# Kernel tuning notes

Measured on AMD Instinct MI355X. Metric: run time of the kernel, lower is better.

## Reference

```python
import jax, jax.numpy as jnp
import numpy as np

B, T, D = 4, 2048, 1024
E, H, K = 8, 2048, 2  # n_expert, expert_dim, top_k


def setup_inputs() -> dict:
    key = jax.random.key(0)
    k1, k2, k3, k4 = jax.random.split(key, 4)
    x = jax.random.normal(k1, (B, T, D), jnp.float32)
    gate_w = jax.random.normal(k2, (D, E), jnp.float32) * 0.02          # Router gate (no bias)
    w1 = jax.random.normal(k3, (E, D, H), jnp.float32) * (1.0 / np.sqrt(D))  # per-expert first Linear
    w2 = jax.random.normal(k4, (E, H, D), jnp.float32) * (1.0 / np.sqrt(H))  # per-expert second Linear
    return {"x": x, "gate_w": gate_w, "w1": w1, "w2": w2}


def reference(x, gate_w, w1, w2):
    b, t, d = x.shape
    xf = x.reshape(-1, d)                                   # [N, D]
    n = xf.shape[0]
    n_expert = gate_w.shape[1]
    # Router
    logits = xf @ gate_w                                    # [N, E]
    probs = jax.nn.softmax(logits, axis=-1)
    topk_probs, topk_idx = jax.lax.top_k(probs, K)          # [N, K]
    topk_probs = topk_probs / jnp.sum(topk_probs, axis=-1, keepdims=True)
    # Dense compute of ALL experts (faithful to original), then gather top-k
    h = jax.nn.gelu(jnp.einsum('nd,edh->neh', xf, w1), approximate=False)  # [N, E, H]
    all_expert_out = jnp.einsum('neh,ehd->ned', h, w2)      # [N, E, D]
    selected = jnp.take_along_axis(all_expert_out, topk_idx[:, :, None], axis=1)  # [N, K, D]
    out = jnp.sum(topk_probs[:, :, None] * selected, axis=1)  # [N, D]  (dropout p=0 -> identity)
    # Load-balancing aux loss
    counts = jnp.zeros((n_expert,), jnp.float32).at[topk_idx.reshape(-1)].add(1.0)
    tokens_per_expert = counts / n
    mean_probs = jnp.mean(probs, axis=0)
    aux_loss = n_expert * jnp.sum(tokens_per_expert * mean_probs)
    return (out.reshape(b, t, d), aux_loss,
            probs.reshape(b, t, n_expert),
            topk_idx.reshape(b, t, K),
            topk_probs.reshape(b, t, K))
```

## Files before the change

### kernel.cpp

```cpp
#include <hip/hip_runtime.h>
#include <hip/hip_bf16.h>
#include <cstdint>

typedef unsigned short u16;
typedef unsigned int u32;
typedef short s16x8 __attribute__((ext_vector_type(8)));
typedef float f32x4 __attribute__((ext_vector_type(4)));

constexpr int NTOK = 8192;
constexpr int DDIM = 1024;
constexpr int NEXP = 8;
constexpr int HDIM = 2048;
constexpr int NPAIR = NTOK * 2;

constexpr size_t OFF_OUT   = 0;
constexpr size_t OFF_AUX   = 8388608;
constexpr size_t OFF_PROBS = 8388609;
constexpr size_t OFF_TIDX  = 8454145;
constexpr size_t OFF_TPR   = 8470529;

constexpr size_t WS_CNT  = 0;
constexpr size_t WS_PSUM = 32;
constexpr size_t WS_IDS  = 1024;
constexpr size_t WS_PRW  = 263168;
constexpr size_t WS_W1T  = 17302528;
constexpr size_t WS_W2T  = 50856960;
constexpr size_t WS_H    = 84411392;
constexpr size_t WS_XB   = 151520256;
constexpr size_t WS_NEED = 168297472;

__device__ __forceinline__ u16 f2b(float f) {
  u32 u = __float_as_uint(f);
  u32 r = (u + 0x7fffu + ((u >> 16) & 1u)) >> 16;
  return (u16)r;
}

typedef const uint32_t __attribute__((address_space(1)))* gptr_t;
typedef uint32_t __attribute__((address_space(3)))* lptr_t;

__device__ __forceinline__ void gload16(const void* gp, void* lp) {
  __builtin_amdgcn_global_load_lds((gptr_t)gp, (lptr_t)(uintptr_t)lp, 16, 0, 0);
}

__global__ __launch_bounds__(256) void prep_kernel(
    const float* __restrict__ x, const float* __restrict__ gw,
    float* __restrict__ outbuf,
    int* __restrict__ cnt, float* __restrict__ psum,
    int* __restrict__ ids, float* __restrict__ prw, u16* __restrict__ xb,
    const float* __restrict__ w1, u16* __restrict__ w1t,
    const float* __restrict__ w2, u16* __restrict__ w2t) {
  __shared__ float smem[DDIM * NEXP];
  __shared__ int lcnt[NEXP];
  __shared__ float psl[NEXP];
  __shared__ int gbl[NEXP];

  const int bid = blockIdx.x;
  const int tid = threadIdx.x;

  if (bid >= 128) {
    int id = bid - 128;
    const float* in;
    u16* out;
    int R, C, e, r;
    if (id < 4096) {
      in = w1; out = w1t; R = DDIM; C = HDIM;
      e = id >> 9; r = id & 511;
    } else {
      id -= 4096;
      in = w2; out = w2t; R = HDIM; C = DDIM;
      e = id >> 9; r = id & 511;
    }
    int xt = (R == DDIM) ? (r & 31) : (r & 15);
    int yt = (R == DDIM) ? (r >> 5) : (r >> 4);
    int c0 = xt * 64, r0 = yt * 64;

    float (*tile)[65] = (float(*)[65])smem;
    int tx = tid & 15, ty = tid >> 4;
    const float* src = in + (size_t)e * R * C;
#pragma unroll
    for (int i = 0; i < 4; ++i) {
      int rr = ty + i * 16;
      float4 v = *(const float4*)(src + (size_t)(r0 + rr) * C + c0 + tx * 4);
      tile[rr][tx * 4 + 0] = v.x; tile[rr][tx * 4 + 1] = v.y;
      tile[rr][tx * 4 + 2] = v.z; tile[rr][tx * 4 + 3] = v.w;
    }
    __syncthreads();
    u16* dst = out + (size_t)e * R * C;
#pragma unroll
    for (int i = 0; i < 4; ++i) {
      int c = ty + i * 16;
      ushort4 o;
      o.x = f2b(tile[tx * 4 + 0][c]); o.y = f2b(tile[tx * 4 + 1][c]);
      o.z = f2b(tile[tx * 4 + 2][c]); o.w = f2b(tile[tx * 4 + 3][c]);
      *(ushort4*)(dst + (size_t)(c0 + c) * R + r0 + tx * 4) = o;
    }
    return;
  }

#pragma unroll
  for (int k = 0; k < 8; ++k)
    ((float4*)smem)[tid + k * 256] = ((const float4*)gw)[tid + k * 256];
  if (tid < NEXP) { lcnt[tid] = 0; psl[tid] = 0.f; }
  __syncthreads();

  const int tloc = tid >> 2, part = tid & 3;
  const int t = bid * 64 + tloc;
  double acc[NEXP];
#pragma unroll
  for (int e = 0; e < NEXP; ++e) acc[e] = 0.0;

  const float* xrow = x + (size_t)t * DDIM + part * 256;
  u16* xbrow = xb + (size_t)t * DDIM + part * 256;
  for (int i = 0; i < 64; ++i) {
    float4 v = ((const float4*)xrow)[i];
    ushort4 o;
    o.x = f2b(v.x); o.y = f2b(v.y); o.z = f2b(v.z); o.w = f2b(v.w);
    ((ushort4*)xbrow)[i] = o;
    const float* g = &smem[(part * 256 + i * 4) * NEXP];
#pragma unroll
    for (int j = 0; j < 4; ++j) {
      double xs = (double)((const float*)&v)[j];
#pragma unroll
      for (int e = 0; e < NEXP; ++e) acc[e] += xs * (double)g[j * NEXP + e];
    }
  }
#pragma unroll
  for (int e = 0; e < NEXP; ++e) {
    acc[e] += __shfl_xor(acc[e], 1);
    acc[e] += __shfl_xor(acc[e], 2);
  }

  int e0 = 0, e1 = 0, lp0 = 0, lp1 = 0;
  float tp0 = 0.f, tp1 = 0.f;
  if (part == 0) {
    float l[NEXP];
#pragma unroll
    for (int e = 0; e < NEXP; ++e) l[e] = (float)acc[e];
    float m = l[0];
#pragma unroll
    for (int e = 1; e < NEXP; ++e) m = fmaxf(m, l[e]);
    float p[NEXP], s = 0.f;
#pragma unroll
    for (int e = 0; e < NEXP; ++e) { p[e] = expf(l[e] - m); s += p[e]; }
    float inv = 1.0f / s;
#pragma unroll
    for (int e = 0; e < NEXP; ++e) {
      p[e] *= inv;
      outbuf[OFF_PROBS + (size_t)t * NEXP + e] = p[e];
      atomicAdd(&psl[e], p[e]);
    }
#pragma unroll
    for (int e = 1; e < NEXP; ++e) if (p[e] > p[e0]) e0 = e;
    e1 = -1;
#pragma unroll
    for (int e = 0; e < NEXP; ++e)
      if (e != e0 && (e1 < 0 || p[e] > p[e1])) e1 = e;
    float ps = p[e0] + p[e1];
    tp0 = p[e0] / ps;
    tp1 = p[e1] / ps;
    outbuf[OFF_TIDX + t * 2 + 0] = (float)e0;
    outbuf[OFF_TIDX + t * 2 + 1] = (float)e1;
    outbuf[OFF_TPR + t * 2 + 0] = tp0;
    outbuf[OFF_TPR + t * 2 + 1] = tp1;
    lp0 = atomicAdd(&lcnt[e0], 1);
    lp1 = atomicAdd(&lcnt[e1], 1);
  }
  __syncthreads();
  if (tid < NEXP) {
    gbl[tid] = atomicAdd(&cnt[tid], lcnt[tid]);
    atomicAdd(&psum[tid], psl[tid]);
  }
  __syncthreads();
  if (part == 0) {
    int pos0 = gbl[e0] + lp0;
    int pos1 = gbl[e1] + lp1;
    ids[e0 * NTOK + pos0] = t;
    ids[e1 * NTOK + pos1] = t;
    prw[e0 * NTOK + pos0] = tp0;
    prw[e1 * NTOK + pos1] = tp1;
  }
}

template <int MODE>
__global__ __launch_bounds__(256, 3) void moe_gemm_kernel(
    const u16* __restrict__ Asrc, const u16* __restrict__ Bt,
    u16* __restrict__ hout, float* __restrict__ yout,
    const int* __restrict__ cnt, const float* __restrict__ psum,
    const int* __restrict__ ids, const float* __restrict__ prw,
    float* __restrict__ outbuf) {
  constexpr int KDIM = (MODE == 0) ? 1024 : 2048;
  constexpr int NDIM = (MODE == 0) ? 2048 : 1024;
  constexpr int NT = KDIM / 32;
  constexpr int NB = NDIM / 128;
  constexpr int MGRP = 4;
  constexpr int QPG = MGRP * NB;
  const int wgid = blockIdx.x;
  const int e = wgid & 7;
  const int q = wgid >> 3;
  const int mg = q / QPG;
  const int r = q % QPG;
  const int m0 = (mg * MGRP + (r % MGRP)) * 128;
  const int n0 = (r / MGRP) * 128;

  int cn[NEXP];
#pragma unroll
  for (int i = 0; i < NEXP; ++i) cn[i] = cnt[i];
  const int cnte = cn[e];

  if (MODE == 0 && wgid == 0 && threadIdx.x == 0) {
    float aux = 0.f;
#pragma unroll
    for (int i = 0; i < NEXP; ++i) aux += (float)cn[i] * psum[i];
    outbuf[OFF_AUX] = aux * (float)NEXP / ((float)NTOK * (float)NTOK);
  }

  if (m0 >= cnte) return;
  int gbase = 0;
#pragma unroll
  for (int i = 0; i < NEXP; ++i) if (i < e) gbase += cn[i];

  __shared__ u16 Al[3][128 * 32];
  __shared__ u16 Bl[3][128 * 32];

  const int tid = threadIdx.x;
  const int lane = tid & 63, wid = tid >> 6;
  const int wm = (wid >> 1) * 64, wn = (wid & 1) * 64;
  const int r15 = lane & 15, l4 = lane >> 4;

  const char* aptr[2];
  const char* bptr[2];
#pragma unroll
  for (int qq = 0; qq < 2; ++qq) {
    int j = qq * 256 + tid;
    int row = j >> 2;
    int c = (j & 3) ^ ((row >> 1) & 3);
    size_t rowoff;
    if (MODE == 0) {
      int mm = m0 + row;
      if (mm > cnte - 1) mm = cnte - 1;
      int tok = ids[e * NTOK + mm];
      rowoff = (size_t)tok * KDIM;
    } else {
      int gr = gbase + m0 + row;
      if (gr > NPAIR - 1) gr = NPAIR - 1;
      rowoff = (size_t)gr * KDIM;
    }
    aptr[qq] = (const char*)Asrc + (rowoff + (size_t)c * 8) * 2;
    size_t nrow = (size_t)e * NDIM + n0 + row;
    bptr[qq] = (const char*)Bt + (nrow * KDIM + (size_t)c * 8) * 2;
  }

  f32x4 acc[4][4];
#pragma unroll
  for (int i = 0; i < 4; ++i)
#pragma unroll
    for (int jn = 0; jn < 4; ++jn) acc[i][jn] = (f32x4){0.f, 0.f, 0.f, 0.f};

#define STAGE(b_, kt_)                                                         \
  do {                                                                         \
    const size_t kofs_ = (size_t)(kt_) * 64;               \
    _Pragma("unroll") for (int qq = 0; qq < 2; ++qq) {                         \
      gload16(aptr[qq] + kofs_, (void*)&Al[b_][(size_t)(qq * 256 + tid) * 8]); \
      gload16(bptr[qq] + kofs_, (void*)&Bl[b_][(size_t)(qq * 256 + tid) * 8]); \
    }                                                                          \
  } while (0)

  auto compute = [&](int b) {
    const s16x8* Av = (const s16x8*)Al[b];
    const s16x8* Bv = (const s16x8*)Bl[b];
    s16x8 af[4], bfr[4];
#pragma unroll
    for (int mi = 0; mi < 4; ++mi) {
      int row = wm + mi * 16 + r15;
      af[mi] = Av[row * 4 + (l4 ^ ((row >> 1) & 3))];
    }
#pragma unroll
    for (int ni = 0; ni < 4; ++ni) {
      int row = wn + ni * 16 + r15;
      bfr[ni] = Bv[row * 4 + (l4 ^ ((row >> 1) & 3))];
    }
#pragma unroll
    for (int mi = 0; mi < 4; ++mi)
#pragma unroll
      for (int ni = 0; ni < 4; ++ni)
        acc[mi][ni] = __builtin_amdgcn_mfma_f32_16x16x32_bf16(
            af[mi], bfr[ni], acc[mi][ni], 0, 0, 0);
  };

  STAGE(0, 0);
  STAGE(1, 1);

  int b0 = 0;
  for (int kt = 0; kt < NT; ++kt) {
    if (kt < NT - 1)
      asm volatile("s_waitcnt vmcnt(4)" ::: "memory");
    else
      asm volatile("s_waitcnt vmcnt(0)" ::: "memory");
    __builtin_amdgcn_s_barrier();
    asm volatile("" ::: "memory");
    if (kt + 2 < NT) {
      int bs = b0 + 2; if (bs >= 3) bs -= 3;
      STAGE(bs, kt + 2);
    }
    compute(b0);
    if (++b0 == 3) b0 = 0;
  }
#undef STAGE

#pragma unroll
  for (int mi = 0; mi < 4; ++mi) {
#pragma unroll
    for (int jr = 0; jr < 4; ++jr) {
      int rl = wm + mi * 16 + l4 * 4 + jr;
      if (m0 + rl < cnte) {
        if (MODE == 0) {
          size_t grow = (size_t)(gbase + m0 + rl);
#pragma unroll
          for (int ni = 0; ni < 4; ++ni) {
            float v = acc[mi][ni][jr];
            v = 0.5f * v * (1.0f + erff(v * 0.70710678118654752f));
            int col = n0 + wn + ni * 16 + r15;
            hout[grow * NDIM + col] = f2b(v);
          }
        } else {
          int tok = ids[e * NTOK + m0 + rl];
          float p = prw[e * NTOK + m0 + rl];
#pragma unroll
          for (int ni = 0; ni < 4; ++ni) {
            int col = n0 + wn + ni * 16 + r15;
            atomicAdd(&yout[(size_t)tok * DDIM + col], p * acc[mi][ni][jr]);
          }
        }
      }
    }
  }
}

extern "C" void kernel_launch(void* const* d_in, const int* in_sizes, int n_in,
                              void* d_out, int out_size, void* d_ws, size_t ws_size,
                              hipStream_t stream) {
  const float* x = (const float*)d_in[0];
  const float* gw = (const float*)d_in[1];
  const float* w1 = (const float*)d_in[2];
  const float* w2 = (const float*)d_in[3];
  float* out = (float*)d_out;
  char* w = (char*)d_ws;
  if (ws_size < WS_NEED) return;

  int* cnt = (int*)(w + WS_CNT);
  float* psum = (float*)(w + WS_PSUM);
  int* ids = (int*)(w + WS_IDS);
  float* prw = (float*)(w + WS_PRW);
  u16* w1t = (u16*)(w + WS_W1T);
  u16* w2t = (u16*)(w + WS_W2T);
  u16* hbuf = (u16*)(w + WS_H);
  u16* xb = (u16*)(w + WS_XB);

  (void)hipMemsetAsync(w, 0, 96, stream);
  (void)hipMemsetAsync(out + OFF_OUT, 0, (size_t)NTOK * DDIM * sizeof(float), stream);
  prep_kernel<<<128 + 8192, 256, 0, stream>>>(x, gw, out, cnt, psum, ids, prw, xb,
                                              w1, w1t, w2, w2t);
  moe_gemm_kernel<0><<<NEXP * 64 * (HDIM / 128), 256, 0, stream>>>(
      xb, w1t, hbuf, nullptr, cnt, psum, ids, prw, out);
  moe_gemm_kernel<1><<<NEXP * 64 * (DDIM / 128), 256, 0, stream>>>(
      hbuf, w2t, nullptr, out + OFF_OUT, cnt, psum, ids, prw, out);
}
```

Baseline: 323.2 us.

## Move w2 transpose into first GEMM launch and fold output zeroing into prep

The w2 fp32-to-bf16 transpose is moved out of the prep kernel and interleaved into the first expert GEMM grid, one transpose block per two GEMM blocks. That way its memory traffic overlaps with compute-bound GEMM work rather than extending prep. The separate memset of the output buffer is replaced by extra zeroing blocks in the prep kernel, which removes one launch. The interleaving raises the GEMM0 grid to 12288 blocks and gives them mixed workloads, which could disturb scheduling and L2 locality.

```diff
diff --git a/kernel.cpp b/kernel.cpp
--- a/kernel.cpp
+++ b/kernel.cpp
@@ -47,8 +47,7 @@
     float* __restrict__ outbuf,
     int* __restrict__ cnt, float* __restrict__ psum,
     int* __restrict__ ids, float* __restrict__ prw, u16* __restrict__ xb,
-    const float* __restrict__ w1, u16* __restrict__ w1t,
-    const float* __restrict__ w2, u16* __restrict__ w2t) {
+    const float* __restrict__ w1, u16* __restrict__ w1t) {
   __shared__ float smem[DDIM * NEXP];
   __shared__ int lcnt[NEXP];
   __shared__ float psl[NEXP];
@@ -57,42 +56,38 @@
   const int bid = blockIdx.x;
   const int tid = threadIdx.x;
 
+  if (bid >= 4224) {
+    float4 z = {0.f, 0.f, 0.f, 0.f};
+    float4* dst = (float4*)(outbuf + OFF_OUT) + (size_t)(bid - 4224) * 4096 + tid;
+#pragma unroll
+    for (int i = 0; i < 16; ++i) dst[i * 256] = z;
+    return;
+  }
+
   if (bid >= 128) {
     int id = bid - 128;
-    const float* in;
-    u16* out;
-    int R, C, e, r;
-    if (id < 4096) {
-      in = w1; out = w1t; R = DDIM; C = HDIM;
-      e = id >> 9; r = id & 511;
-    } else {
-      id -= 4096;
-      in = w2; out = w2t; R = HDIM; C = DDIM;
-      e = id >> 9; r = id & 511;
-    }
-    int xt = (R == DDIM) ? (r & 31) : (r & 15);
-    int yt = (R == DDIM) ? (r >> 5) : (r >> 4);
-    int c0 = xt * 64, r0 = yt * 64;
+    int e = id >> 9, r = id & 511;
+    int c0 = (r & 31) * 64, r0 = (r >> 5) * 64;
 
     float (*tile)[65] = (float(*)[65])smem;
     int tx = tid & 15, ty = tid >> 4;
-    const float* src = in + (size_t)e * R * C;
+    const float* src = w1 + (size_t)e * DDIM * HDIM;
 #pragma unroll
     for (int i = 0; i < 4; ++i) {
       int rr = ty + i * 16;
-      float4 v = *(const float4*)(src + (size_t)(r0 + rr) * C + c0 + tx * 4);
+      float4 v = *(const float4*)(src + (size_t)(r0 + rr) * HDIM + c0 + tx * 4);
       tile[rr][tx * 4 + 0] = v.x; tile[rr][tx * 4 + 1] = v.y;
       tile[rr][tx * 4 + 2] = v.z; tile[rr][tx * 4 + 3] = v.w;
     }
     __syncthreads();
-    u16* dst = out + (size_t)e * R * C;
+    u16* dst = w1t + (size_t)e * DDIM * HDIM;
 #pragma unroll
     for (int i = 0; i < 4; ++i) {
       int c = ty + i * 16;
       ushort4 o;
       o.x = f2b(tile[tx * 4 + 0][c]); o.y = f2b(tile[tx * 4 + 1][c]);
       o.z = f2b(tile[tx * 4 + 2][c]); o.w = f2b(tile[tx * 4 + 3][c]);
-      *(ushort4*)(dst + (size_t)(c0 + c) * R + r0 + tx * 4) = o;
+      *(ushort4*)(dst + (size_t)(c0 + c) * DDIM + r0 + tx * 4) = o;
     }
     return;
   }
@@ -187,16 +182,55 @@
     u16* __restrict__ hout, float* __restrict__ yout,
     const int* __restrict__ cnt, const float* __restrict__ psum,
     const int* __restrict__ ids, const float* __restrict__ prw,
-    float* __restrict__ outbuf) {
+    float* __restrict__ outbuf,
+    const float* __restrict__ w2, u16* __restrict__ w2t) {
   constexpr int KDIM = (MODE == 0) ? 1024 : 2048;
   constexpr int NDIM = (MODE == 0) ? 2048 : 1024;
   constexpr int NT = KDIM / 32;
   constexpr int NB = NDIM / 128;
   constexpr int MGRP = 4;
   constexpr int QPG = MGRP * NB;
+
+  __shared__ u16 Al[3][128 * 32];
+  __shared__ u16 Bl[3][128 * 32];
+
   const int wgid = blockIdx.x;
-  const int e = wgid & 7;
-  const int q = wgid >> 3;
+  const int tid = threadIdx.x;
+  int gid;
+  if (MODE == 0) {
+    int g3 = wgid / 3, r3 = wgid - g3 * 3;
+    if (r3 == 2) {
+      int e = g3 >> 9, r = g3 & 511;
+      int c0 = (r & 15) * 64, r0 = (r >> 4) * 64;
+      float (*tile)[65] = (float(*)[65])Al;
+      int tx = tid & 15, ty = tid >> 4;
+      const float* src = w2 + (size_t)e * HDIM * DDIM;
+#pragma unroll
+      for (int i = 0; i < 4; ++i) {
+        int rr = ty + i * 16;
+        float4 v = *(const float4*)(src + (size_t)(r0 + rr) * DDIM + c0 + tx * 4);
+        tile[rr][tx * 4 + 0] = v.x; tile[rr][tx * 4 + 1] = v.y;
+        tile[rr][tx * 4 + 2] = v.z; tile[rr][tx * 4 + 3] = v.w;
+      }
+      __syncthreads();
+      u16* dst = w2t + (size_t)e * HDIM * DDIM;
+#pragma unroll
+      for (int i = 0; i < 4; ++i) {
+        int c = ty + i * 16;
+        ushort4 o;
+        o.x = f2b(tile[tx * 4 + 0][c]); o.y = f2b(tile[tx * 4 + 1][c]);
+        o.z = f2b(tile[tx * 4 + 2][c]); o.w = f2b(tile[tx * 4 + 3][c]);
+        *(ushort4*)(dst + (size_t)(c0 + c) * HDIM + r0 + tx * 4) = o;
+      }
+      return;
+    }
+    gid = g3 * 2 + r3;
+  } else {
+    gid = wgid;
+  }
+
+  const int e = gid & 7;
+  const int q = gid >> 3;
   const int mg = q / QPG;
   const int r = q % QPG;
   const int m0 = (mg * MGRP + (r % MGRP)) * 128;
@@ -207,7 +241,7 @@
   for (int i = 0; i < NEXP; ++i) cn[i] = cnt[i];
   const int cnte = cn[e];
 
-  if (MODE == 0 && wgid == 0 && threadIdx.x == 0) {
+  if (MODE == 0 && gid == 0 && tid == 0) {
     float aux = 0.f;
 #pragma unroll
     for (int i = 0; i < NEXP; ++i) aux += (float)cn[i] * psum[i];
@@ -219,10 +253,6 @@
 #pragma unroll
   for (int i = 0; i < NEXP; ++i) if (i < e) gbase += cn[i];
 
-  __shared__ u16 Al[3][128 * 32];
-  __shared__ u16 Bl[3][128 * 32];
-
-  const int tid = threadIdx.x;
   const int lane = tid & 63, wid = tid >> 6;
   const int wm = (wid >> 1) * 64, wn = (wid & 1) * 64;
   const int r15 = lane & 15, l4 = lane >> 4;
@@ -357,11 +387,9 @@
   u16* xb = (u16*)(w + WS_XB);
 
   (void)hipMemsetAsync(w, 0, 96, stream);
-  (void)hipMemsetAsync(out + OFF_OUT, 0, (size_t)NTOK * DDIM * sizeof(float), stream);
-  prep_kernel<<<128 + 8192, 256, 0, stream>>>(x, gw, out, cnt, psum, ids, prw, xb,
-                                              w1, w1t, w2, w2t);
-  moe_gemm_kernel<0><<<NEXP * 64 * (HDIM / 128), 256, 0, stream>>>(
-      xb, w1t, hbuf, nullptr, cnt, psum, ids, prw, out);
+  prep_kernel<<<4736, 256, 0, stream>>>(x, gw, out, cnt, psum, ids, prw, xb, w1, w1t);
+  moe_gemm_kernel<0><<<12288, 256, 0, stream>>>(
+      xb, w1t, hbuf, nullptr, cnt, psum, ids, prw, out, w2, w2t);
   moe_gemm_kernel<1><<<NEXP * 64 * (DDIM / 128), 256, 0, stream>>>(
-      hbuf, w2t, nullptr, out + OFF_OUT, cnt, psum, ids, prw, out);
-}
+      hbuf, w2t, nullptr, out + OFF_OUT, cnt, psum, ids, prw, out, nullptr, nullptr);
+}
```

After: 300.0 us (median of 3 runs). 7.2% less time.
